# Kernel optimization log

Hardware: AMD Instinct MI355X
Metric: run time of the kernel (lower is better)

The kernel has to match this reference:

```python
import jax, jax.numpy as jnp
import numpy as np

EMB = 1024
HEADS = 16
HEAD_DIM = EMB // HEADS
ROPE_BASE = 10000.0


def rotate_half(x):
    # Interleaved rotate: pairs (x0,x1,x2,x3,...) -> (-x1,x0,-x3,x2,...)
    x1 = x[..., ::2]
    x2 = x[..., 1::2]
    return jnp.stack((-x2, x1), axis=-1).reshape(x.shape)


def rope_cos_sin(seq_len, head_dim):
    inv_freq = 1.0 / (ROPE_BASE ** (jnp.arange(0, head_dim, 2, dtype=jnp.float32) / head_dim))
    pos = jnp.arange(seq_len, dtype=jnp.float32)
    freqs = jnp.outer(pos, inv_freq)            # [S, hd/2]
    emb = jnp.concatenate([freqs, freqs], -1)   # [S, hd]  (NOTE: concat, matching source)
    return jnp.cos(emb)[None, None], jnp.sin(emb)[None, None]  # [1,1,S,hd]


def setup_inputs() -> dict:
    key = jax.random.key(0)
    ks = jax.random.split(key, 5)
    B, S = 2, 2048
    x = jax.random.normal(ks[0], (B, S, EMB), dtype=jnp.float32)
    scale = EMB ** -0.5
    Wq = jax.random.normal(ks[1], (EMB, EMB), dtype=jnp.float32) * scale
    Wk = jax.random.normal(ks[2], (EMB, EMB), dtype=jnp.float32) * scale
    Wv = jax.random.normal(ks[3], (EMB, EMB), dtype=jnp.float32) * scale
    Wo = jax.random.normal(ks[4], (EMB, EMB), dtype=jnp.float32) * scale
    return {"x": x, "Wq": Wq, "Wk": Wk, "Wv": Wv, "Wo": Wo}


def reference(x, Wq, Wk, Wv, Wo):
    B, S, E = x.shape
    def shape_heads(t):
        return t.reshape(B, S, HEADS, HEAD_DIM).transpose(0, 2, 1, 3)  # [B,H,S,hd]
    q = shape_heads(x @ Wq.T)
    k = shape_heads(x @ Wk.T)
    v = shape_heads(x @ Wv.T)
    cos, sin = rope_cos_sin(S, HEAD_DIM)
    q = q * cos + rotate_half(q) * sin
    k = k * cos + rotate_half(k) * sin
    scale = HEAD_DIM ** -0.5
    scores = jnp.einsum('bhqd,bhkd->bhqk', q, k) * scale  # [B,H,S,S]
    causal = jnp.triu(jnp.ones((S, S), dtype=bool), k=1)
    scores = jnp.where(causal, -jnp.inf, scores)
    attn = jax.nn.softmax(scores, axis=-1)
    out = jnp.einsum('bhqk,bhkd->bhqd', attn, v)           # [B,H,S,hd]
    out = out.transpose(0, 2, 1, 3).reshape(B, S, E)
    return out @ Wo.T
```

## Files before the change

kernel.cpp:

```cpp
#include <hip/hip_runtime.h>
#include <cstdint>
#include <cstddef>

typedef __bf16 bf16;
typedef __attribute__((ext_vector_type(8))) __bf16 bf16x8;
typedef __attribute__((ext_vector_type(4))) __bf16 bf16x4;
typedef __attribute__((ext_vector_type(4))) float f32x4;

constexpr int kS = 2048;
constexpr int kH = 16;
constexpr int kD = 64;

__device__ __forceinline__ void gload16(const bf16* g, bf16* l) {
  __builtin_amdgcn_global_load_lds((const __attribute__((address_space(1))) void*)g,
                                   (__attribute__((address_space(3))) void*)l, 16, 0, 0);
}

__global__ __launch_bounds__(256) void cast_all_kernel(
    const float* __restrict__ x, const float* __restrict__ wq, const float* __restrict__ wk,
    const float* __restrict__ wv, const float* __restrict__ wo,
    bf16* __restrict__ xb, bf16* __restrict__ wqb, bf16* __restrict__ wkb,
    bf16* __restrict__ wvb, bf16* __restrict__ wob) {
  int idx = blockIdx.x * 256 + threadIdx.x;
  const float* src; bf16* dst; int i;
  if (idx < (1 << 20)) { src = x; dst = xb; i = idx << 2; }
  else {
    int r = idx - (1 << 20);
    int t = r >> 18;
    i = (r & ((1 << 18) - 1)) << 2;
    src = (t == 0) ? wq : (t == 1) ? wk : (t == 2) ? wv : wo;
    dst = (t == 0) ? wqb : (t == 1) ? wkb : (t == 2) ? wvb : wob;
  }
  float4 v = *(const float4*)(src + i);
  bf16x4 o;
  o[0] = (bf16)v.x; o[1] = (bf16)v.y; o[2] = (bf16)v.z; o[3] = (bf16)v.w;
  *(bf16x4*)(dst + i) = o;
}


#define GSTAGE(BUF, KT)                                    \
  gload16(aP0 + (KT), &As[BUF][(w * 64 + l) * 8]);         \
  gload16(aP1 + (KT), &As[BUF][((4 + w) * 64 + l) * 8]);   \
  gload16(bP0 + (KT), &Bs[BUF][(w * 64 + l) * 8]);         \
  gload16(bP1 + (KT), &Bs[BUF][((4 + w) * 64 + l) * 8]);

__global__ __launch_bounds__(256) void gemm_qkv(const bf16* __restrict__ A,
                                                const bf16* __restrict__ wq,
                                                const bf16* __restrict__ wk,
                                                const bf16* __restrict__ wv,
                                                bf16* __restrict__ qo,
                                                bf16* __restrict__ ko,
                                                bf16* __restrict__ vto) {
  __shared__ bf16 As[2][128 * 32];
  __shared__ bf16 Bs[2][128 * 32];
  const int tid = threadIdx.x;
  const int w = tid >> 6, l = tid & 63;
  const int wr = w >> 1, wc = w & 1;
  const int lr = l & 15, lg = l >> 4;

  const int fid = (blockIdx.x & 7) * 96 + (blockIdx.x >> 3);
  const int mblk = fid & 31;
  const int ntile = fid >> 5;
  const int which = ntile >> 3;
  const int m0 = mblk * 128;
  const int n0 = (ntile & 7) * 128;
  const bf16* Bw = (which == 0) ? wq : (which == 1) ? wk : wv;

  const int srow = l >> 2;
  const int skcol = ((l & 3) ^ ((l >> 3) & 3)) << 3;
  const int K = 1024;

  const bf16* aP0 = A + (size_t)(m0 + w * 16 + srow) * K + skcol;
  const bf16* aP1 = A + (size_t)(m0 + 64 + w * 16 + srow) * K + skcol;
  const bf16* bP0 = Bw + (size_t)(n0 + w * 16 + srow) * K + skcol;
  const bf16* bP1 = Bw + (size_t)(n0 + 64 + w * 16 + srow) * K + skcol;

  f32x4 acc[4][4] = {};
  const int ca = (lg ^ ((lr >> 1) & 3)) * 8;

  GSTAGE(0, 0)
  __syncthreads();
  int cur = 0;
  for (int kt = 0; kt < K; kt += 32) {
    if (kt + 32 < K) { GSTAGE(cur ^ 1, kt + 32) }
    bf16x8 af[4], bfg[4];
#pragma unroll
    for (int mi = 0; mi < 4; mi++)
      af[mi] = *(const bf16x8*)&As[cur][(wr * 64 + mi * 16 + lr) * 32 + ca];
#pragma unroll
    for (int ni = 0; ni < 4; ni++)
      bfg[ni] = *(const bf16x8*)&Bs[cur][(wc * 64 + ni * 16 + lr) * 32 + ca];
    __builtin_amdgcn_s_setprio(1);
#pragma unroll
    for (int mi = 0; mi < 4; mi++)
#pragma unroll
      for (int ni = 0; ni < 4; ni++)
        acc[mi][ni] = __builtin_amdgcn_mfma_f32_16x16x32_bf16(af[mi], bfg[ni], acc[mi][ni], 0, 0, 0);
    __builtin_amdgcn_s_setprio(0);
    __syncthreads();
    cur ^= 1;
  }

  float invf_[4];
#pragma unroll
  for (int ni = 0; ni < 4; ni++) {
    int d31 = ((n0 + wc * 64 + ni * 16 + lr) & 63) & 31;
    invf_[ni] = exp2f((float)d31 * -0.41524100480466348f);
  }

#pragma unroll
  for (int mi = 0; mi < 4; mi++) {
#pragma unroll
    for (int ni = 0; ni < 4; ni++) {
#pragma unroll
      for (int r = 0; r < 4; r++) {
        const int m = m0 + wr * 64 + mi * 16 + lg * 4 + r;
        const int n = n0 + wc * 64 + ni * 16 + lr;
        float v = acc[mi][ni][r];
        const int st = m & 2047;
        const size_t bh = (size_t)(m >> 11) * kH + (n >> 6);
        if (which < 2) {
          float vp = __shfl_xor(v, 1);
          const int d = n & 63;
          float th = (float)st * invf_[ni];
          float sth = __sinf(th), cth = __cosf(th);
          float rv = v * cth + ((d & 1) ? vp : -vp) * sth;
          bf16* dst = which ? ko : qo;
          dst[((bh << 11) + st) * kD + (n & 63)] = (bf16)rv;
        } else {
          int pos = (st & ~31) | (((st >> 2) & 3) << 3) | (((st >> 4) & 1) << 2) | (st & 3);
          vto[((bh * kD + (n & 63)) << 11) + pos] = (bf16)v;
        }
      }
    }
  }
}

__global__ __launch_bounds__(256) void gemm_out(const bf16* __restrict__ A,
                                                const bf16* __restrict__ Bw,
                                                float* __restrict__ Cout) {
  __shared__ bf16 As[2][128 * 32];
  __shared__ bf16 Bs[2][128 * 32];
  const int tid = threadIdx.x;
  const int w = tid >> 6, l = tid & 63;
  const int wr = w >> 1, wc = w & 1;
  const int lr = l & 15, lg = l >> 4;
  const int m0 = blockIdx.y * 128, n0 = blockIdx.x * 128;
  const int K = 1024, N = 1024;

  const int srow = l >> 2;
  const int skcol = ((l & 3) ^ ((l >> 3) & 3)) << 3;

  const bf16* aP0 = A + (size_t)(m0 + w * 16 + srow) * K + skcol;
  const bf16* aP1 = A + (size_t)(m0 + 64 + w * 16 + srow) * K + skcol;
  const bf16* bP0 = Bw + (size_t)(n0 + w * 16 + srow) * K + skcol;
  const bf16* bP1 = Bw + (size_t)(n0 + 64 + w * 16 + srow) * K + skcol;

  f32x4 acc[4][4] = {};
  const int ca = (lg ^ ((lr >> 1) & 3)) * 8;

  GSTAGE(0, 0)
  __syncthreads();
  int cur = 0;
  for (int kt = 0; kt < K; kt += 32) {
    if (kt + 32 < K) { GSTAGE(cur ^ 1, kt + 32) }
    bf16x8 af[4], bfg[4];
#pragma unroll
    for (int mi = 0; mi < 4; mi++)
      af[mi] = *(const bf16x8*)&As[cur][(wr * 64 + mi * 16 + lr) * 32 + ca];
#pragma unroll
    for (int ni = 0; ni < 4; ni++)
      bfg[ni] = *(const bf16x8*)&Bs[cur][(wc * 64 + ni * 16 + lr) * 32 + ca];
    __builtin_amdgcn_s_setprio(1);
#pragma unroll
    for (int mi = 0; mi < 4; mi++)
#pragma unroll
      for (int ni = 0; ni < 4; ni++)
        acc[mi][ni] = __builtin_amdgcn_mfma_f32_16x16x32_bf16(af[mi], bfg[ni], acc[mi][ni], 0, 0, 0);
    __builtin_amdgcn_s_setprio(0);
    __syncthreads();
    cur ^= 1;
  }

#pragma unroll
  for (int mi = 0; mi < 4; mi++)
#pragma unroll
    for (int ni = 0; ni < 4; ni++)
#pragma unroll
      for (int r = 0; r < 4; r++) {
        const int m = m0 + wr * 64 + mi * 16 + lg * 4 + r;
        const int n = n0 + wc * 64 + ni * 16 + lr;
        Cout[(size_t)m * N + n] = acc[mi][ni][r];
      }
}


#define STAGE(BUF, KV0)                                                                  \
  {                                                                                      \
    const bf16* kg_ = kh + (size_t)((KV0) + w * 16 + lr) * 64 + lg * 8;                  \
    gload16(kg_,      &Ks[BUF][(w * 2 + 0) * 512 + l * 8]);                              \
    gload16(kg_ + 32, &Ks[BUF][(w * 2 + 1) * 512 + l * 8]);                              \
    const bf16* vg_ = vh + (size_t)(w * 16 + lr) * 2048 + (KV0) + lg * 8;                \
    gload16(vg_,      &Vs[BUF][(w * 2 + 0) * 512 + l * 8]);                              \
    gload16(vg_ + 32, &Vs[BUF][(w * 2 + 1) * 512 + l * 8]);                              \
  }

#define COMPUTE(BUF, DIAG, O, LPART, QF, QROW, KVB)                                      \
  {                                                                                      \
    bf16x8 kf_[4][2], vf_[4][2];                                                         \
    _Pragma("unroll") for (int s_ = 0; s_ < 4; s_++)                                     \
      _Pragma("unroll") for (int c_ = 0; c_ < 2; c_++)                                   \
        kf_[s_][c_] = *(const bf16x8*)&Ks[BUF][(s_ * 2 + c_) * 512 + l * 8];             \
    _Pragma("unroll") for (int c_ = 0; c_ < 4; c_++)                                     \
      _Pragma("unroll") for (int f_ = 0; f_ < 2; f_++)                                   \
        vf_[c_][f_] = *(const bf16x8*)&Vs[BUF][(c_ * 2 + f_) * 512 + l * 8];             \
    f32x4 sa_[4] = {};                                                                   \
    __builtin_amdgcn_s_setprio(1);                                                       \
    _Pragma("unroll") for (int s_ = 0; s_ < 4; s_++) {                                   \
      sa_[s_] = __builtin_amdgcn_mfma_f32_16x16x32_bf16(kf_[s_][0], QF[0], sa_[s_], 0, 0, 0); \
      sa_[s_] = __builtin_amdgcn_mfma_f32_16x16x32_bf16(kf_[s_][1], QF[1], sa_[s_], 0, 0, 0); \
    }                                                                                    \
    __builtin_amdgcn_s_setprio(0);                                                       \
    bf16x8 pf_[2];                                                                       \
    float sum0_ = 0.0f, sum1_ = 0.0f;                                                    \
    _Pragma("unroll") for (int s_ = 0; s_ < 4; s_++)                                     \
      _Pragma("unroll") for (int r_ = 0; r_ < 4; r_++) {                                 \
        float sc_ = fmaf(sa_[s_][r_], 0.1803368801111244f, -11.541560327111707f);        \
        if (DIAG) {                                                                      \
          int kk_ = (KVB) + s_ * 16 + lg * 4 + r_;                                       \
          sc_ = (kk_ <= (QROW)) ? sc_ : -1e30f;                                          \
        }                                                                                \
        float e_ = exp2f(sc_);                                                           \
        if (s_ & 1) sum1_ += e_; else sum0_ += e_;                                       \
        pf_[s_ >> 1][(s_ & 1) * 4 + r_] = (bf16)e_;                                      \
      }                                                                                  \
    LPART += sum0_ + sum1_;                                                              \
    __builtin_amdgcn_s_setprio(1);                                                       \
    _Pragma("unroll") for (int c_ = 0; c_ < 4; c_++) {                                   \
      O[c_] = __builtin_amdgcn_mfma_f32_16x16x32_bf16(vf_[c_][0], pf_[0], O[c_], 0, 0, 0); \
      O[c_] = __builtin_amdgcn_mfma_f32_16x16x32_bf16(vf_[c_][1], pf_[1], O[c_], 0, 0, 0); \
    }                                                                                    \
    __builtin_amdgcn_s_setprio(0);                                                       \
  }

#define EPILOG(O, LPART, Q0)                                                             \
  {                                                                                      \
    float lt_ = LPART;                                                                   \
    lt_ += __shfl_xor(lt_, 16);                                                          \
    lt_ += __shfl_xor(lt_, 32);                                                          \
    const float inv_ = 1.0f / lt_;                                                       \
    _Pragma("unroll") for (int c_ = 0; c_ < 4; c_++) {                                   \
      bf16x4 ov_;                                                                        \
      _Pragma("unroll") for (int r_ = 0; r_ < 4; r_++) ov_[r_] = (bf16)(O[c_][r_] * inv_); \
      size_t addr_ = ((size_t)(b * kS + (Q0) + lr)) * (kH * kD) + h * 64 + c_ * 16 + lg * 4; \
      *(bf16x4*)&ob[addr_] = ov_;                                                        \
    }                                                                                    \
  }

__global__ __launch_bounds__(256, 4) void attn_kernel(const bf16* __restrict__ qb,
                                                      const bf16* __restrict__ kb,
                                                      const bf16* __restrict__ vtb,
                                                      bf16* __restrict__ ob) {
  __shared__ bf16 Ks[2][4096];
  __shared__ bf16 Vs[2][4096];
  const int tid = threadIdx.x;
  const int w = tid >> 6, l = tid & 63;
  const int lr = l & 15, lg = l >> 4;
  const int bid = blockIdx.x;
  const int bh = bid & 31;
  const int qt = 31 - (bid >> 5);
  const bf16* qh = qb + (size_t)bh * (kS * kD);
  const bf16* kh = kb + (size_t)bh * (kS * kD);
  const bf16* vh = vtb + (size_t)bh * (kS * kD);
  const int b = bh >> 4, h = bh & 15;

  const int q0 = qt * 64 + w * 16;
  const int q = q0 + lr;
  bf16x8 qf[2];
#pragma unroll
  for (int c = 0; c < 2; c++)
    qf[c] = *(const bf16x8*)&qh[(size_t)(q0 + lr) * kD + c * 32 + lg * 8];

  float lpart = 0.0f;
  f32x4 o[4] = {};

  STAGE(0, 0)
  __syncthreads();
  int cur = 0;
  for (int t = 0; t <= qt; t++) {
    if (t < qt) STAGE(cur ^ 1, (t + 1) * 64)
    COMPUTE(cur, (t == qt), o, lpart, qf, q, t * 64)
    __syncthreads();
    cur ^= 1;
  }
  EPILOG(o, lpart, q0)
}

extern "C" void kernel_launch(void* const* d_in, const int* in_sizes, int n_in,
                              void* d_out, int out_size, void* d_ws, size_t ws_size,
                              hipStream_t stream) {
  const float* x  = (const float*)d_in[0];
  const float* wq = (const float*)d_in[1];
  const float* wk = (const float*)d_in[2];
  const float* wv = (const float*)d_in[3];
  const float* wo = (const float*)d_in[4];

  bf16* xb  = (bf16*)d_ws;
  bf16* qb  = xb + (1 << 22);
  bf16* kb  = qb + (1 << 22);
  bf16* vtb = kb + (1 << 22);
  bf16* ab  = vtb + (1 << 22);
  bf16* wqb = ab + (1 << 22);
  bf16* wkb = wqb + (1 << 20);
  bf16* wvb = wkb + (1 << 20);
  bf16* wob = wvb + (1 << 20);

  cast_all_kernel<<<8192, 256, 0, stream>>>(x, wq, wk, wv, wo, xb, wqb, wkb, wvb, wob);
  gemm_qkv<<<768, 256, 0, stream>>>(xb, wqb, wkb, wvb, qb, kb, vtb);
  attn_kernel<<<1024, 256, 0, stream>>>(qb, kb, vtb, ab);
  gemm_out<<<dim3(8, 32), 256, 0, stream>>>(ab, wob, (float*)d_out);
}
```

Before: 130.3 us.

## Process two 16-row query blocks per wave to reuse staged K/V tiles

Each attention block now handles 128 query rows instead of 64, with every wave computing two 16-row query sub-blocks against each staged K/V tile. This halves the grid and the K/V global loads and LDS staging per query row, and reuses the K/V fragments read from LDS across both sub-blocks. In exchange it doubles the accumulator registers (launch bounds lowered to 2 blocks per CU), applies the causal mask over the last two tiles, and coarsens causal load balance with fewer, larger blocks.

```diff
diff --git a/kernel.cpp b/kernel.cpp
--- a/kernel.cpp
+++ b/kernel.cpp
@@ -205,7 +205,7 @@
     gload16(vg_ + 32, &Vs[BUF][(w * 2 + 1) * 512 + l * 8]);                              \
   }
 
-#define COMPUTE(BUF, DIAG, O, LPART, QF, QROW, KVB)                                      \
+#define COMPUTE2(BUF, DIAG, KVB)                                                         \
   {                                                                                      \
     bf16x8 kf_[4][2], vf_[4][2];                                                         \
     _Pragma("unroll") for (int s_ = 0; s_ < 4; s_++)                                     \
@@ -214,50 +214,52 @@
     _Pragma("unroll") for (int c_ = 0; c_ < 4; c_++)                                     \
       _Pragma("unroll") for (int f_ = 0; f_ < 2; f_++)                                   \
         vf_[c_][f_] = *(const bf16x8*)&Vs[BUF][(c_ * 2 + f_) * 512 + l * 8];             \
-    f32x4 sa_[4] = {};                                                                   \
-    __builtin_amdgcn_s_setprio(1);                                                       \
-    _Pragma("unroll") for (int s_ = 0; s_ < 4; s_++) {                                   \
-      sa_[s_] = __builtin_amdgcn_mfma_f32_16x16x32_bf16(kf_[s_][0], QF[0], sa_[s_], 0, 0, 0); \
-      sa_[s_] = __builtin_amdgcn_mfma_f32_16x16x32_bf16(kf_[s_][1], QF[1], sa_[s_], 0, 0, 0); \
+    _Pragma("unroll") for (int qb_ = 0; qb_ < 2; qb_++) {                                \
+      f32x4 sa_[4] = {};                                                                 \
+      __builtin_amdgcn_s_setprio(1);                                                     \
+      _Pragma("unroll") for (int s_ = 0; s_ < 4; s_++) {                                 \
+        sa_[s_] = __builtin_amdgcn_mfma_f32_16x16x32_bf16(kf_[s_][0], qf[qb_][0], sa_[s_], 0, 0, 0); \
+        sa_[s_] = __builtin_amdgcn_mfma_f32_16x16x32_bf16(kf_[s_][1], qf[qb_][1], sa_[s_], 0, 0, 0); \
+      }                                                                                  \
+      __builtin_amdgcn_s_setprio(0);                                                     \
+      bf16x8 pf_[2];                                                                     \
+      float sum0_ = 0.0f, sum1_ = 0.0f;                                                  \
+      _Pragma("unroll") for (int s_ = 0; s_ < 4; s_++)                                   \
+        _Pragma("unroll") for (int r_ = 0; r_ < 4; r_++) {                               \
+          float sc_ = fmaf(sa_[s_][r_], 0.1803368801111244f, -11.541560327111707f);      \
+          if (DIAG) {                                                                    \
+            int kk_ = (KVB) + s_ * 16 + lg * 4 + r_;                                     \
+            sc_ = (kk_ <= q_[qb_]) ? sc_ : -1e30f;                                       \
+          }                                                                              \
+          float e_ = exp2f(sc_);                                                         \
+          if (s_ & 1) sum1_ += e_; else sum0_ += e_;                                     \
+          pf_[s_ >> 1][(s_ & 1) * 4 + r_] = (bf16)e_;                                    \
+        }                                                                                \
+      lp[qb_] += sum0_ + sum1_;                                                          \
+      __builtin_amdgcn_s_setprio(1);                                                     \
+      _Pragma("unroll") for (int c_ = 0; c_ < 4; c_++) {                                 \
+        o[qb_][c_] = __builtin_amdgcn_mfma_f32_16x16x32_bf16(vf_[c_][0], pf_[0], o[qb_][c_], 0, 0, 0); \
+        o[qb_][c_] = __builtin_amdgcn_mfma_f32_16x16x32_bf16(vf_[c_][1], pf_[1], o[qb_][c_], 0, 0, 0); \
+      }                                                                                  \
+      __builtin_amdgcn_s_setprio(0);                                                     \
     }                                                                                    \
-    __builtin_amdgcn_s_setprio(0);                                                       \
-    bf16x8 pf_[2];                                                                       \
-    float sum0_ = 0.0f, sum1_ = 0.0f;                                                    \
-    _Pragma("unroll") for (int s_ = 0; s_ < 4; s_++)                                     \
-      _Pragma("unroll") for (int r_ = 0; r_ < 4; r_++) {                                 \
-        float sc_ = fmaf(sa_[s_][r_], 0.1803368801111244f, -11.541560327111707f);        \
-        if (DIAG) {                                                                      \
-          int kk_ = (KVB) + s_ * 16 + lg * 4 + r_;                                       \
-          sc_ = (kk_ <= (QROW)) ? sc_ : -1e30f;                                          \
-        }                                                                                \
-        float e_ = exp2f(sc_);                                                           \
-        if (s_ & 1) sum1_ += e_; else sum0_ += e_;                                       \
-        pf_[s_ >> 1][(s_ & 1) * 4 + r_] = (bf16)e_;                                      \
-      }                                                                                  \
-    LPART += sum0_ + sum1_;                                                              \
-    __builtin_amdgcn_s_setprio(1);                                                       \
-    _Pragma("unroll") for (int c_ = 0; c_ < 4; c_++) {                                   \
-      O[c_] = __builtin_amdgcn_mfma_f32_16x16x32_bf16(vf_[c_][0], pf_[0], O[c_], 0, 0, 0); \
-      O[c_] = __builtin_amdgcn_mfma_f32_16x16x32_bf16(vf_[c_][1], pf_[1], O[c_], 0, 0, 0); \
-    }                                                                                    \
-    __builtin_amdgcn_s_setprio(0);                                                       \
-  }
-
-#define EPILOG(O, LPART, Q0)                                                             \
+  }
+
+#define EPILOG(QB, Q0)                                                                   \
   {                                                                                      \
-    float lt_ = LPART;                                                                   \
+    float lt_ = lp[QB];                                                                  \
     lt_ += __shfl_xor(lt_, 16);                                                          \
     lt_ += __shfl_xor(lt_, 32);                                                          \
     const float inv_ = 1.0f / lt_;                                                       \
     _Pragma("unroll") for (int c_ = 0; c_ < 4; c_++) {                                   \
       bf16x4 ov_;                                                                        \
-      _Pragma("unroll") for (int r_ = 0; r_ < 4; r_++) ov_[r_] = (bf16)(O[c_][r_] * inv_); \
+      _Pragma("unroll") for (int r_ = 0; r_ < 4; r_++) ov_[r_] = (bf16)(o[QB][c_][r_] * inv_); \
       size_t addr_ = ((size_t)(b * kS + (Q0) + lr)) * (kH * kD) + h * 64 + c_ * 16 + lg * 4; \
       *(bf16x4*)&ob[addr_] = ov_;                                                        \
     }                                                                                    \
   }
 
-__global__ __launch_bounds__(256, 4) void attn_kernel(const bf16* __restrict__ qb,
+__global__ __launch_bounds__(256, 2) void attn_kernel(const bf16* __restrict__ qb,
                                                       const bf16* __restrict__ kb,
                                                       const bf16* __restrict__ vtb,
                                                       bf16* __restrict__ ob) {
@@ -268,32 +270,38 @@
   const int lr = l & 15, lg = l >> 4;
   const int bid = blockIdx.x;
   const int bh = bid & 31;
-  const int qt = 31 - (bid >> 5);
+  const int qt = 15 - (bid >> 5);
   const bf16* qh = qb + (size_t)bh * (kS * kD);
   const bf16* kh = kb + (size_t)bh * (kS * kD);
   const bf16* vh = vtb + (size_t)bh * (kS * kD);
   const int b = bh >> 4, h = bh & 15;
 
-  const int q0 = qt * 64 + w * 16;
-  const int q = q0 + lr;
-  bf16x8 qf[2];
-#pragma unroll
-  for (int c = 0; c < 2; c++)
-    qf[c] = *(const bf16x8*)&qh[(size_t)(q0 + lr) * kD + c * 32 + lg * 8];
-
-  float lpart = 0.0f;
-  f32x4 o[4] = {};
+  const int q0 = qt * 128 + w * 32;
+  int q_[2];
+  bf16x8 qf[2][2];
+#pragma unroll
+  for (int qb_ = 0; qb_ < 2; qb_++) {
+    q_[qb_] = q0 + qb_ * 16 + lr;
+#pragma unroll
+    for (int c = 0; c < 2; c++)
+      qf[qb_][c] = *(const bf16x8*)&qh[(size_t)(q0 + qb_ * 16 + lr) * kD + c * 32 + lg * 8];
+  }
+
+  float lp[2] = {0.0f, 0.0f};
+  f32x4 o[2][4] = {};
+  const int ntiles = (qt + 1) * 2;
 
   STAGE(0, 0)
   __syncthreads();
   int cur = 0;
-  for (int t = 0; t <= qt; t++) {
-    if (t < qt) STAGE(cur ^ 1, (t + 1) * 64)
-    COMPUTE(cur, (t == qt), o, lpart, qf, q, t * 64)
+  for (int t = 0; t < ntiles; t++) {
+    if (t + 1 < ntiles) STAGE(cur ^ 1, (t + 1) * 64)
+    COMPUTE2(cur, (t + 2 >= ntiles), t * 64)
     __syncthreads();
     cur ^= 1;
   }
-  EPILOG(o, lpart, q0)
+  EPILOG(0, q0)
+  EPILOG(1, q0 + 16)
 }
 
 extern "C" void kernel_launch(void* const* d_in, const int* in_sizes, int n_in,
@@ -317,6 +325,6 @@
 
   cast_all_kernel<<<8192, 256, 0, stream>>>(x, wq, wk, wv, wo, xb, wqb, wkb, wvb, wob);
   gemm_qkv<<<768, 256, 0, stream>>>(xb, wqb, wkb, wvb, qb, kb, vtb);
-  attn_kernel<<<1024, 256, 0, stream>>>(qb, kb, vtb, ab);
+  attn_kernel<<<512, 256, 0, stream>>>(qb, kb, vtb, ab);
   gemm_out<<<dim3(8, 32), 256, 0, stream>>>(ab, wob, (float*)d_out);
 }
```

Result: slower. 149.1 us (+14.4%).

## Retile QKV GEMM to 256x256 blocks and fold softmax scale into K

Applied to the files above, without the earlier changes.

The QKV projection GEMM moves from 128x128 tiles with 256 threads to 256x256 tiles with 512 threads (8 waves, each computing 128x64). This raises data reuse per LDS load and cuts the grid from 768 to 192 blocks. The softmax scale (log2e/sqrt(d)) is now applied to K in the GEMM epilogue, so the attention inner loop no longer needs its per-score FMA. The attention loop also drops the constant max-offset subtraction, which risks exp2 overflow for large scores. The smaller grid may leave many compute units idle on a 256-CU device.

```diff
diff --git a/kernel.cpp b/kernel.cpp
--- a/kernel.cpp
+++ b/kernel.cpp
@@ -38,61 +38,61 @@
 }
 
 
-#define GSTAGE(BUF, KT)                                    \
-  gload16(aP0 + (KT), &As[BUF][(w * 64 + l) * 8]);         \
-  gload16(aP1 + (KT), &As[BUF][((4 + w) * 64 + l) * 8]);   \
-  gload16(bP0 + (KT), &Bs[BUF][(w * 64 + l) * 8]);         \
-  gload16(bP1 + (KT), &Bs[BUF][((4 + w) * 64 + l) * 8]);
-
-__global__ __launch_bounds__(256) void gemm_qkv(const bf16* __restrict__ A,
+__global__ __launch_bounds__(512) void gemm_qkv(const bf16* __restrict__ A,
                                                 const bf16* __restrict__ wq,
                                                 const bf16* __restrict__ wk,
                                                 const bf16* __restrict__ wv,
                                                 bf16* __restrict__ qo,
                                                 bf16* __restrict__ ko,
                                                 bf16* __restrict__ vto) {
-  __shared__ bf16 As[2][128 * 32];
-  __shared__ bf16 Bs[2][128 * 32];
+  __shared__ bf16 As[2][256 * 32];
+  __shared__ bf16 Bs[2][256 * 32];
   const int tid = threadIdx.x;
   const int w = tid >> 6, l = tid & 63;
-  const int wr = w >> 1, wc = w & 1;
+  const int wr = w >> 2, wc = w & 3;
   const int lr = l & 15, lg = l >> 4;
 
-  const int fid = (blockIdx.x & 7) * 96 + (blockIdx.x >> 3);
-  const int mblk = fid & 31;
-  const int ntile = fid >> 5;
-  const int which = ntile >> 3;
-  const int m0 = mblk * 128;
-  const int n0 = (ntile & 7) * 128;
+  const int fid = (blockIdx.x & 7) * 24 + (blockIdx.x >> 3);
+  const int mblk = fid & 15;
+  const int ntile = fid >> 4;
+  const int which = ntile >> 2;
+  const int m0 = mblk * 256;
+  const int n0g = (ntile & 3) * 256;
   const bf16* Bw = (which == 0) ? wq : (which == 1) ? wk : wv;
 
   const int srow = l >> 2;
   const int skcol = ((l & 3) ^ ((l >> 3) & 3)) << 3;
   const int K = 1024;
 
-  const bf16* aP0 = A + (size_t)(m0 + w * 16 + srow) * K + skcol;
-  const bf16* aP1 = A + (size_t)(m0 + 64 + w * 16 + srow) * K + skcol;
-  const bf16* bP0 = Bw + (size_t)(n0 + w * 16 + srow) * K + skcol;
-  const bf16* bP1 = Bw + (size_t)(n0 + 64 + w * 16 + srow) * K + skcol;
-
-  f32x4 acc[4][4] = {};
+  const bf16* aP0 = A + (size_t)(m0 + w * 32 + srow) * K + skcol;
+  const bf16* aP1 = aP0 + (size_t)16 * K;
+  const bf16* bP0 = Bw + (size_t)(n0g + w * 32 + srow) * K + skcol;
+  const bf16* bP1 = bP0 + (size_t)16 * K;
+
+  f32x4 acc[8][4] = {};
   const int ca = (lg ^ ((lr >> 1) & 3)) * 8;
 
-  GSTAGE(0, 0)
+#define QSTAGE(BUF, KT)                                        \
+  gload16(aP0 + (KT), &As[BUF][((w * 2 + 0) * 64 + l) * 8]);   \
+  gload16(aP1 + (KT), &As[BUF][((w * 2 + 1) * 64 + l) * 8]);   \
+  gload16(bP0 + (KT), &Bs[BUF][((w * 2 + 0) * 64 + l) * 8]);   \
+  gload16(bP1 + (KT), &Bs[BUF][((w * 2 + 1) * 64 + l) * 8]);
+
+  QSTAGE(0, 0)
   __syncthreads();
   int cur = 0;
   for (int kt = 0; kt < K; kt += 32) {
-    if (kt + 32 < K) { GSTAGE(cur ^ 1, kt + 32) }
-    bf16x8 af[4], bfg[4];
-#pragma unroll
-    for (int mi = 0; mi < 4; mi++)
-      af[mi] = *(const bf16x8*)&As[cur][(wr * 64 + mi * 16 + lr) * 32 + ca];
+    if (kt + 32 < K) { QSTAGE(cur ^ 1, kt + 32) }
+    bf16x8 af[8], bfg[4];
+#pragma unroll
+    for (int mi = 0; mi < 8; mi++)
+      af[mi] = *(const bf16x8*)&As[cur][(wr * 128 + mi * 16 + lr) * 32 + ca];
 #pragma unroll
     for (int ni = 0; ni < 4; ni++)
       bfg[ni] = *(const bf16x8*)&Bs[cur][(wc * 64 + ni * 16 + lr) * 32 + ca];
     __builtin_amdgcn_s_setprio(1);
 #pragma unroll
-    for (int mi = 0; mi < 4; mi++)
+    for (int mi = 0; mi < 8; mi++)
 #pragma unroll
       for (int ni = 0; ni < 4; ni++)
         acc[mi][ni] = __builtin_amdgcn_mfma_f32_16x16x32_bf16(af[mi], bfg[ni], acc[mi][ni], 0, 0, 0);
@@ -104,37 +104,45 @@
   float invf_[4];
 #pragma unroll
   for (int ni = 0; ni < 4; ni++) {
-    int d31 = ((n0 + wc * 64 + ni * 16 + lr) & 63) & 31;
+    int d31 = (ni * 16 + lr) & 31;
     invf_[ni] = exp2f((float)d31 * -0.41524100480466348f);
   }
 
 #pragma unroll
-  for (int mi = 0; mi < 4; mi++) {
+  for (int mi = 0; mi < 8; mi++) {
 #pragma unroll
     for (int ni = 0; ni < 4; ni++) {
 #pragma unroll
       for (int r = 0; r < 4; r++) {
-        const int m = m0 + wr * 64 + mi * 16 + lg * 4 + r;
-        const int n = n0 + wc * 64 + ni * 16 + lr;
+        const int m = m0 + wr * 128 + mi * 16 + lg * 4 + r;
+        const int nt = n0g + wc * 64 + ni * 16 + lr;
         float v = acc[mi][ni][r];
         const int st = m & 2047;
-        const size_t bh = (size_t)(m >> 11) * kH + (n >> 6);
+        const size_t bh = (size_t)(m >> 11) * kH + (nt >> 6);
         if (which < 2) {
           float vp = __shfl_xor(v, 1);
-          const int d = n & 63;
+          const int d = nt & 63;
           float th = (float)st * invf_[ni];
           float sth = __sinf(th), cth = __cosf(th);
           float rv = v * cth + ((d & 1) ? vp : -vp) * sth;
+          if (which == 1) rv *= 0.18033688011112042f;
           bf16* dst = which ? ko : qo;
-          dst[((bh << 11) + st) * kD + (n & 63)] = (bf16)rv;
+          dst[((bh << 11) + st) * kD + d] = (bf16)rv;
         } else {
           int pos = (st & ~31) | (((st >> 2) & 3) << 3) | (((st >> 4) & 1) << 2) | (st & 3);
-          vto[((bh * kD + (n & 63)) << 11) + pos] = (bf16)v;
+          vto[((bh * kD + (nt & 63)) << 11) + pos] = (bf16)v;
         }
       }
     }
   }
-}
+#undef QSTAGE
+}
+
+#define GSTAGE(BUF, KT)                                    \
+  gload16(aP0 + (KT), &As[BUF][(w * 64 + l) * 8]);         \
+  gload16(aP1 + (KT), &As[BUF][((4 + w) * 64 + l) * 8]);   \
+  gload16(bP0 + (KT), &Bs[BUF][(w * 64 + l) * 8]);         \
+  gload16(bP1 + (KT), &Bs[BUF][((4 + w) * 64 + l) * 8]);
 
 __global__ __launch_bounds__(256) void gemm_out(const bf16* __restrict__ A,
                                                 const bf16* __restrict__ Bw,
@@ -225,7 +233,7 @@
     float sum0_ = 0.0f, sum1_ = 0.0f;                                                    \
     _Pragma("unroll") for (int s_ = 0; s_ < 4; s_++)                                     \
       _Pragma("unroll") for (int r_ = 0; r_ < 4; r_++) {                                 \
-        float sc_ = fmaf(sa_[s_][r_], 0.1803368801111244f, -11.541560327111707f);        \
+        float sc_ = sa_[s_][r_];                                                         \
         if (DIAG) {                                                                      \
           int kk_ = (KVB) + s_ * 16 + lg * 4 + r_;                                       \
           sc_ = (kk_ <= (QROW)) ? sc_ : -1e30f;                                          \
@@ -316,7 +324,7 @@
   bf16* wob = wvb + (1 << 20);
 
   cast_all_kernel<<<8192, 256, 0, stream>>>(x, wq, wk, wv, wo, xb, wqb, wkb, wvb, wob);
-  gemm_qkv<<<768, 256, 0, stream>>>(xb, wqb, wkb, wvb, qb, kb, vtb);
+  gemm_qkv<<<192, 512, 0, stream>>>(xb, wqb, wkb, wvb, qb, kb, vtb);
   attn_kernel<<<1024, 256, 0, stream>>>(qb, kb, vtb, ab);
   gemm_out<<<dim3(8, 32), 256, 0, stream>>>(ab, wob, (float*)d_out);
 }
```

New measurement: 147.7 us. 1.13x slower.
